# Kernel tuning notes

Hardware: AMD Instinct MI355X
Metric: run time of the kernel (lower is better)

The kernel has to match this reference:

```python
import jax, jax.numpy as jnp
import numpy as np

B, A, N, P, D, H = 2, 9, 1024, 4, 256, 8
DH = D // H
EPS = 1e-12


def _layernorm(x, gamma, beta):
    m = jnp.mean(x, axis=-1, keepdims=True)
    v = jnp.var(x, axis=-1, keepdims=True)
    return (x - m) / jnp.sqrt(v + EPS) * gamma + beta


def setup_inputs() -> dict:
    key = jax.random.key(0)
    ks = jax.random.split(key, 10)
    # adjacency stacks A relation matrices; scale 1/N keeps the P-step matmul chain O(1)
    adjacency = jax.random.uniform(ks[0], (B, A, N, N), jnp.float32) / N
    # diagonal, strictly positive degree matrix -> invertible
    diag = 1.0 + jax.random.uniform(ks[1], (B, N), jnp.float32)
    degree = jax.vmap(jnp.diag)(diag)
    x = jax.random.normal(ks[2], (B, N, D), jnp.float32)
    # per-head params stacked on leading H axis
    kernels = 0.1 * jax.random.normal(ks[3], (H, A, P), jnp.float32)  # RandomNormal(0, 0.1)
    lim = np.sqrt(6.0 / D).astype(np.float32)
    Wv = jax.random.uniform(ks[4], (H, D, DH), jnp.float32, -lim, lim)  # he_uniform
    Bv = jnp.zeros((H, N, DH), jnp.float32)
    W0 = jax.random.uniform(ks[5], (D, D), jnp.float32, -lim, lim)
    gamma2 = jnp.ones((D,), jnp.float32)
    beta2 = jnp.zeros((D,), jnp.float32)
    W1 = jax.random.normal(ks[6], (D, 2 * D), jnp.float32) * np.sqrt(2.0 / D).astype(np.float32)
    b1 = jnp.zeros((2 * D,), jnp.float32)
    gf = jnp.ones((2 * D,), jnp.float32)
    bf = jnp.zeros((2 * D,), jnp.float32)
    W2 = jax.random.normal(ks[7], (2 * D, D), jnp.float32) * np.sqrt(2.0 / (2 * D)).astype(np.float32)
    b2f = jnp.zeros((D,), jnp.float32)
    return {"adjacency": adjacency, "degree": degree, "x": x, "kernels": kernels,
            "Wv": Wv, "Bv": Bv, "W0": W0, "gamma2": gamma2, "beta2": beta2,
            "W1": W1, "b1": b1, "gf": gf, "bf": bf, "W2": W2, "b2f": b2f}


def reference(adjacency, degree, x, kernels, Wv, Bv, W0, gamma2, beta2, W1, b1, gf, bf, W2, b2f):
    # ---- AdjacencyAggregator (all H heads batched on leading axis) ----
    # softmax(relu(kernel)) over the input-channel (relation) axis
    soft = jax.nn.softmax(jax.nn.relu(kernels), axis=-2)  # [H, A, P]
    # 1x1 conv == per-position convex mix of the A relation matrices, one mix per path step
    # sequential chain: meta = M_0 @ M_1 @ ... @ M_{P-1}   (P is small and fixed)
    result = jnp.einsum('banm,ha->hbnm', adjacency, soft[:, :, 0])  # [H, B, N, N]
    for i in range(1, P):
        mi = jnp.einsum('banm,ha->hbnm', adjacency, soft[:, :, i])
        result = jnp.matmul(result, mi)
    inv_deg = jnp.linalg.inv(degree)                # [B, N, N], shared across heads
    normed = jnp.matmul(inv_deg[None], result)      # [H, B, N, N]
    # ---- MetaPathHead value projection + message passing ----
    V = jnp.einsum('bnd,hde->hbne', x, Wv) + Bv[:, None]   # [H, B, N, DH]
    heads = jnp.matmul(normed, V)                          # [H, B, N, DH]
    # concat along feature axis in head order
    attn = jnp.transpose(heads, (1, 2, 0, 3)).reshape(B, N, D)
    # ---- outer block: W0, residual, pre-norm FFN ----
    residual = attn @ W0 + x
    h = _layernorm(residual, gamma2, beta2)
    f = jax.nn.gelu(h @ W1 + b1, approximate=False)
    f = _layernorm(f, gf, bf)
    out = f @ W2 + b2f + residual
    return out
```

## Files before the change

kernel.cpp:

```cpp
#include <hip/hip_runtime.h>
#include <hip/hip_bf16.h>
#include <math.h>

#define B_ 2
#define A_ 9
#define N_ 1024
#define P_ 4
#define D_ 256
#define H_ 8
#define DH_ 32
#define ROWS_ (B_*N_)
#define KS_ 8
#define ADJ_ELEMS_ ((size_t)B_*A_*N_*N_)
#define SLABF4_ 131072

typedef __attribute__((ext_vector_type(8))) short bf16x8;
typedef __attribute__((ext_vector_type(4))) float f32x4;

__device__ __forceinline__ uint pack2_bf(float x, float y) {
    uint ux = __float_as_uint(x); ux += 0x7fffu + ((ux >> 16) & 1u);
    uint uy = __float_as_uint(y); uy += 0x7fffu + ((uy >> 16) & 1u);
    return (ux >> 16) | (uy & 0xffff0000u);
}
__device__ __forceinline__ float bflo(uint u){ return __uint_as_float(u << 16); }
__device__ __forceinline__ float bfhi(uint u){ return __uint_as_float(u & 0xffff0000u); }

__global__ void prep_kernel(const float* __restrict__ kernels, const float* __restrict__ degree,
                            float* __restrict__ soft, float* __restrict__ invd)
{
    int t = threadIdx.x;
    if (blockIdx.x == 0) {
        if (t < H_*P_) {
            int h = t >> 2, p = t & 3;
            float vals[A_];
            float m = 0.0f;
            #pragma unroll
            for (int a = 0; a < A_; a++) {
                float v = kernels[h*A_*P_ + a*P_ + p];
                v = v > 0.0f ? v : 0.0f;
                vals[a] = v;
                m = fmaxf(m, v);
            }
            float s = 0.0f;
            #pragma unroll
            for (int a = 0; a < A_; a++) { vals[a] = expf(vals[a] - m); s += vals[a]; }
            float inv = 1.0f / s;
            #pragma unroll
            for (int a = 0; a < A_; a++) soft[h*A_*P_ + a*P_ + p] = vals[a] * inv;
        }
    } else {
        int idx = (blockIdx.x - 1) * 256 + t;
        if (idx < ROWS_) {
            int b = idx >> 10, n = idx & (N_-1);
            invd[idx] = 1.0f / degree[(size_t)b*N_*N_ + (size_t)n*N_ + n];
        }
    }
}

__global__ void adj_pack_kernel(const float* __restrict__ in, ushort* __restrict__ out)
{
    int j = blockIdx.x * 256 + threadIdx.x;
    int kk8   = j & 3;
    int r     = (j >> 2) & 15;
    int t     = j >> 6;
    int a     = t % 9;
    int rest  = t / 9;
    int chunk = rest & 3;
    int ks    = (rest >> 2) & 7;
    int rowblk= (rest >> 5) & 63;
    int b     = rest >> 11;
    const float* src = &in[(((size_t)b*A_ + a)*N_ + (rowblk*16 + r))*N_ + ks*128 + chunk*32 + kk8*8];
    float4 v0 = *(const float4*)src;
    float4 v1 = *(const float4*)(src + 4);
    uint4 o;
    o.x = pack2_bf(v0.x, v0.y);
    o.y = pack2_bf(v0.z, v0.w);
    o.z = pack2_bf(v1.x, v1.y);
    o.w = pack2_bf(v1.z, v1.w);
    ((uint4*)out)[j] = o;
}

__global__ __launch_bounds__(256, 4)
void chain_mfma(const ushort* __restrict__ adjp, const float* __restrict__ soft,
                const ushort* __restrict__ Tin, float* __restrict__ Pp, int step)
{
    __shared__ __align__(16) ushort smem[8*640 + 16*648];
    __shared__ float soft_s[8][9];
    ushort* sm_ms = smem;
    ushort* sm_t  = smem + 8*640;

    int bid    = blockIdx.x;
    int ks     = bid & (KS_-1);
    int rowblk = (bid >> 3) & 63;
    int b      = bid >> 9;
    int n0     = rowblk * 16;
    int tid    = threadIdx.x;
    int lane   = tid & 63;
    int w      = tid >> 6;

    if (tid < 72) { int h = tid/9, a = tid%9; soft_s[h][a] = soft[h*A_*P_ + a*P_ + step]; }
    __syncthreads();

    int mr   = tid >> 4;
    int mk2  = (tid & 15) * 2;
    int mk2s = mk2 ^ ((mr & 3) << 3);
    const ushort* ablk = adjp + (size_t)((b*64 + rowblk)*8 + ks) * 18432;

    int sp  = tid >> 4;
    int sk0 = (tid & 15) * 2;
    const ushort* tbase = Tin + ((size_t)(b*16 + sp)*1024 + (size_t)ks*128) * 16;

    int g   = lane >> 4;
    int c15 = lane & 15;
    int gx  = (g ^ (c15 & 3)) * 8;

    f32x4 acc[4];
    #pragma unroll
    for (int j = 0; j < 4; j++) acc[j] = (f32x4){0.f, 0.f, 0.f, 0.f};

    for (int chunk = 0; chunk < 4; chunk++) {
        uint av[9];
        {
            const ushort* asl = ablk + chunk*4608 + mk2;
            #pragma unroll
            for (int a = 0; a < A_; a++) av[a] = *(const uint*)&asl[(a*16 + mr)*32];
        }
        const ushort* tsl = tbase + (size_t)(chunk*32 + sk0) * 16;
        uint4 q0 = *(const uint4*)(tsl + 0);
        uint4 q1 = *(const uint4*)(tsl + 8);
        uint4 q2 = *(const uint4*)(tsl + 16);
        uint4 q3 = *(const uint4*)(tsl + 24);

        if (chunk) __syncthreads();

        {
            float va0[9], va1[9];
            #pragma unroll
            for (int a = 0; a < A_; a++) { va0[a] = bflo(av[a]); va1[a] = bfhi(av[a]); }
            #pragma unroll
            for (int h = 0; h < H_; h++) {
                float s0 = soft_s[h][0]*va0[0];
                float s1 = soft_s[h][0]*va1[0];
                #pragma unroll
                for (int a = 1; a < A_; a++) { s0 += soft_s[h][a]*va0[a]; s1 += soft_s[h][a]*va1[a]; }
                *(uint*)&sm_ms[h*640 + mr*40 + mk2s] = pack2_bf(s0, s1);
            }
        }
        {
            uint l0[4] = {q0.x, q0.y, q0.z, q0.w};
            uint l1[4] = {q1.x, q1.y, q1.z, q1.w};
            uint h0[4] = {q2.x, q2.y, q2.z, q2.w};
            uint h1[4] = {q3.x, q3.y, q3.z, q3.w};
            #pragma unroll
            for (int ci = 0; ci < 8; ci++) {
                uint a0 = (l0[ci>>1] >> ((ci&1)*16)) & 0xffffu;
                uint b0 = (h0[ci>>1] >> ((ci&1)*16)) & 0xffffu;
                int k0s = sk0 ^ ((ci & 3) << 3);
                *(uint*)&sm_t[sp*648 + ci*40 + k0s] = a0 | (b0 << 16);
            }
            #pragma unroll
            for (int ci = 0; ci < 8; ci++) {
                int c = ci + 8;
                uint a0 = (l1[ci>>1] >> ((ci&1)*16)) & 0xffffu;
                uint b0 = (h1[ci>>1] >> ((ci&1)*16)) & 0xffffu;
                int k0s = sk0 ^ ((c & 3) << 3);
                *(uint*)&sm_t[sp*648 + c*40 + k0s] = a0 | (b0 << 16);
            }
        }
        __syncthreads();

        {
            const ushort* mb = sm_ms + c15*40 + gx;
            const ushort* tb = sm_t  + c15*40 + gx;
            #pragma unroll
            for (int j = 0; j < 4; j++) {
                int cg = w + 4*j;
                int h  = cg >> 1;
                bf16x8 af  = *(const bf16x8*)&mb[h*640];
                bf16x8 bfr = *(const bf16x8*)&tb[cg*648];
                acc[j] = __builtin_amdgcn_mfma_f32_16x16x32_bf16(af, bfr, acc[j], 0, 0, 0);
            }
        }
    }

    __syncthreads();
    float* Ep = (float*)smem;
    #pragma unroll
    for (int j = 0; j < 4; j++) {
        int cg = w + 4*j;
        #pragma unroll
        for (int i = 0; i < 4; i++)
            Ep[cg*256 + (g*4 + i)*16 + c15] = acc[j][i];
    }
    __syncthreads();
    {
        int p = tid >> 4, r = tid & 15;
        float* dst = Pp + (((size_t)(ks*B_ + b)*16 + p)*N_ + (n0 + r)) * 16;
        const float* src = &Ep[p*256 + r*16];
        *(float4*)&dst[0]  = *(const float4*)&src[0];
        *(float4*)&dst[4]  = *(const float4*)&src[4];
        *(float4*)&dst[8]  = *(const float4*)&src[8];
        *(float4*)&dst[12] = *(const float4*)&src[12];
    }
}

template<int FINAL>
__global__ void chain_reduce(const float* __restrict__ Pp, ushort* __restrict__ outp,
                             const float* __restrict__ invd)
{
    int pidx = blockIdx.x * 256 + threadIdx.x;
    float4 s = make_float4(0.f, 0.f, 0.f, 0.f);
    #pragma unroll
    for (int ks = 0; ks < KS_; ks++) {
        float4 v = ((const float4*)Pp)[(size_t)ks*SLABF4_ + pidx];
        s.x += v.x; s.y += v.y; s.z += v.z; s.w += v.w;
    }
    if constexpr (FINAL) {
        int lin = pidx * 4;
        int n  = (lin >> 4) & (N_-1);
        int b  = lin >> 18;
        float sc = invd[b*N_ + n];
        s.x *= sc; s.y *= sc; s.z *= sc; s.w *= sc;
    }
    uint2 wv;
    wv.x = pack2_bf(s.x, s.y);
    wv.y = pack2_bf(s.z, s.w);
    ((uint2*)outp)[pidx] = wv;
}

#define BK 16
__global__ void gemm_v(const float* __restrict__ A, const float* __restrict__ Bm,
                       const float* __restrict__ bias, ushort* __restrict__ C)
{
    __shared__ __align__(16) float As[BK][68];
    __shared__ __align__(16) float Bs[BK][68];
    int m0 = blockIdx.x * 64;
    int n0 = blockIdx.y * 64;
    int tid = threadIdx.x;
    int tx = tid & 15, ty = tid >> 4;

    float acc[4][4];
    #pragma unroll
    for (int i = 0; i < 4; i++)
        #pragma unroll
        for (int j = 0; j < 4; j++) acc[i][j] = 0.0f;

    for (int k0 = 0; k0 < D_; k0 += BK) {
        {
            int m = tid >> 2;
            int k = (tid & 3) * 4;
            float4 v = *(const float4*)&A[(size_t)(m0+m)*D_ + k0 + k];
            As[k+0][m] = v.x; As[k+1][m] = v.y; As[k+2][m] = v.z; As[k+3][m] = v.w;
        }
        {
            int k = tid >> 4;
            int n = (tid & 15) * 4;
            int c = n0 + n; int h = c >> 5; int ee = c & 31;
            float4 v = *(const float4*)&Bm[(size_t)h*D_*DH_ + (size_t)(k0+k)*DH_ + ee];
            *(float4*)&Bs[k][n] = v;
        }
        __syncthreads();
        #pragma unroll
        for (int k = 0; k < BK; k++) {
            float4 a4 = *(const float4*)&As[k][ty*4];
            float4 b4 = *(const float4*)&Bs[k][tx*4];
            acc[0][0] += a4.x*b4.x; acc[0][1] += a4.x*b4.y; acc[0][2] += a4.x*b4.z; acc[0][3] += a4.x*b4.w;
            acc[1][0] += a4.y*b4.x; acc[1][1] += a4.y*b4.y; acc[1][2] += a4.y*b4.z; acc[1][3] += a4.y*b4.w;
            acc[2][0] += a4.z*b4.x; acc[2][1] += a4.z*b4.y; acc[2][2] += a4.z*b4.z; acc[2][3] += a4.z*b4.w;
            acc[3][0] += a4.w*b4.x; acc[3][1] += a4.w*b4.y; acc[3][2] += a4.w*b4.z; acc[3][3] += a4.w*b4.w;
        }
        __syncthreads();
    }

    #pragma unroll
    for (int i = 0; i < 4; i++) {
        int row  = m0 + ty*4 + i;
        int nloc = n0 + tx*4;
        float o[4];
        #pragma unroll
        for (int j = 0; j < 4; j++) {
            int c = nloc + j;
            int h = c >> 5, ee = c & 31, n = row & (N_-1);
            o[j] = acc[i][j] + bias[(size_t)h*N_*DH_ + (size_t)n*DH_ + ee];
        }
        int bb = row >> 10, n = row & (N_-1);
        int cg = nloc >> 4, cc = nloc & 15;
        uint2 wv;
        wv.x = pack2_bf(o[0], o[1]);
        wv.y = pack2_bf(o[2], o[3]);
        *(uint2*)&C[(((size_t)bb*16 + cg)*N_ + n)*16 + cc] = wv;
    }
}


__global__ __launch_bounds__(256, 2)
void gemm_r(const ushort* __restrict__ attnp, const float* __restrict__ W0,
            const float* __restrict__ x, const float* __restrict__ gamma,
            const float* __restrict__ beta, float* __restrict__ resid,
            ushort* __restrict__ hbuf)
{
    __shared__ __align__(16) ushort As[16*40];
    __shared__ __align__(16) ushort Bs[256*40];
    __shared__ float lnb[16*257];
    __shared__ float2 stat[16];

    int m0 = blockIdx.x * 16;
    int b16 = (m0 >> 10) * 16;
    int nb  = m0 & (N_-1);
    int tid = threadIdx.x;
    int lane = tid & 63;
    int w = tid >> 6;
    int g = lane >> 4, c15 = lane & 15;
    int gx = (g ^ (c15 & 3)) * 8;

    int am = tid >> 4, ak2 = (tid & 15) * 2;
    int apos = am*40 + ((((ak2>>3) ^ (am&3))) << 3) + (ak2 & 7);
    int bn8 = (tid & 31) * 8;
    int bkq = (tid >> 5) * 4;
    int bpos0 = (((bkq>>3)) << 3) + (bkq & 7);

    f32x4 acc[4];
    #pragma unroll
    for (int j = 0; j < 4; j++) acc[j] = (f32x4){0.f,0.f,0.f,0.f};

    for (int ks = 0; ks < 8; ks++) {
        int k0 = ks * 32;
        int k = k0 + ak2;
        uint av = *(const uint*)&attnp[(((size_t)(b16 + (k>>4)))*N_ + nb + am)*16 + (k & 15)];
        float4 lo[4], hi[4];
        #pragma unroll
        for (int i = 0; i < 4; i++) {
            lo[i] = *(const float4*)&W0[(size_t)(k0+bkq+i)*D_ + bn8];
            hi[i] = *(const float4*)&W0[(size_t)(k0+bkq+i)*D_ + bn8 + 4];
        }
        if (ks) __syncthreads();
        *(uint*)&As[apos] = av;
        #pragma unroll
        for (int jn = 0; jn < 8; jn++) {
            int n = bn8 + jn;
            float v0 = (jn<4)? ((const float*)&lo[0])[jn] : ((const float*)&hi[0])[jn-4];
            float v1 = (jn<4)? ((const float*)&lo[1])[jn] : ((const float*)&hi[1])[jn-4];
            float v2 = (jn<4)? ((const float*)&lo[2])[jn] : ((const float*)&hi[2])[jn-4];
            float v3 = (jn<4)? ((const float*)&lo[3])[jn] : ((const float*)&hi[3])[jn-4];
            uint2 wv; wv.x = pack2_bf(v0, v1); wv.y = pack2_bf(v2, v3);
            *(uint2*)&Bs[n*40 + (bpos0 ^ ((n&3)<<3))] = wv;
        }
        __syncthreads();
        const ushort* ab = As + c15*40 + gx;
        #pragma unroll
        for (int nt = 0; nt < 4; nt++) {
            int n = w*64 + nt*16 + c15;
            bf16x8 af  = *(const bf16x8*)ab;
            bf16x8 bfr = *(const bf16x8*)&Bs[n*40 + gx];
            acc[nt] = __builtin_amdgcn_mfma_f32_16x16x32_bf16(af, bfr, acc[nt], 0, 0, 0);
        }
    }
    __syncthreads();

    #pragma unroll
    for (int nt = 0; nt < 4; nt++) {
        int c = w*64 + nt*16 + c15;
        #pragma unroll
        for (int i = 0; i < 4; i++) {
            int r = g*4 + i;
            lnb[r*257 + c] = acc[nt][i] + x[(size_t)(m0+r)*D_ + c];
        }
    }
    __syncthreads();

    {
        int rr = tid >> 4, sl = tid & 15;
        float sum = 0.f, sq = 0.f;
        #pragma unroll
        for (int j = 0; j < 16; j++) {
            float v = lnb[rr*257 + sl + 16*j];
            sum += v; sq += v*v;
        }
        #pragma unroll
        for (int m = 1; m < 16; m <<= 1) { sum += __shfl_xor(sum, m); sq += __shfl_xor(sq, m); }
        if (sl == 0) {
            float mean = sum * (1.0f/D_);
            float var  = fmaxf(sq * (1.0f/D_) - mean*mean, 0.f);
            stat[rr] = make_float2(mean, rsqrtf(var + 1e-12f));
        }
    }
    __syncthreads();

    {
        int rr = tid & 15, s2 = tid >> 4;
        float2 ms = stat[rr];
        int c0 = s2 * 16;
        uint hw[8];
        #pragma unroll
        for (int q = 0; q < 4; q++) {
            int c = c0 + q*4;
            float4 v = *(const float4*)&lnb[rr*257 + c];
            *(float4*)&resid[(size_t)(m0+rr)*D_ + c] = v;
            float4 gm = *(const float4*)&gamma[c];
            float4 bt = *(const float4*)&beta[c];
            float h0 = (v.x - ms.x)*ms.y*gm.x + bt.x;
            float h1 = (v.y - ms.x)*ms.y*gm.y + bt.y;
            float h2 = (v.z - ms.x)*ms.y*gm.z + bt.z;
            float h3 = (v.w - ms.x)*ms.y*gm.w + bt.w;
            hw[2*q]   = pack2_bf(h0, h1);
            hw[2*q+1] = pack2_bf(h2, h3);
        }
        ushort* hp = &hbuf[(size_t)(m0+rr)*D_ + c0];
        *(uint4*)&hp[0] = make_uint4(hw[0], hw[1], hw[2], hw[3]);
        *(uint4*)&hp[8] = make_uint4(hw[4], hw[5], hw[6], hw[7]);
    }
}

__global__ __launch_bounds__(256, 2)
void gemm_f1(const ushort* __restrict__ hbuf, const float* __restrict__ W1,
             const float* __restrict__ b1, const float* __restrict__ gf,
             const float* __restrict__ bfv, ushort* __restrict__ fout)
{
    __shared__ __align__(16) ushort As[16*40];
    __shared__ __align__(16) ushort Bs[512*40];
    __shared__ float lnb[16*513];
    __shared__ float2 stat[16];

    int m0 = blockIdx.x * 16;
    int tid = threadIdx.x;
    int lane = tid & 63;
    int w = tid >> 6;
    int g = lane >> 4, c15 = lane & 15;
    int gx = (g ^ (c15 & 3)) * 8;

    int am = tid >> 4, ak2 = (tid & 15) * 2;
    int apos = am*40 + ((((ak2>>3) ^ (am&3))) << 3) + (ak2 & 7);
    int bn8 = (tid & 63) * 8;
    int bk8 = (tid >> 6) * 8;

    f32x4 acc[8];
    #pragma unroll
    for (int j = 0; j < 8; j++) acc[j] = (f32x4){0.f,0.f,0.f,0.f};

    for (int ks = 0; ks < 8; ks++) {
        int k0 = ks * 32;
        uint av = *(const uint*)&hbuf[(size_t)(m0+am)*D_ + k0 + ak2];
        float4 q[16];
        #pragma unroll
        for (int i = 0; i < 8; i++) {
            q[2*i]   = *(const float4*)&W1[(size_t)(k0+bk8+i)*(2*D_) + bn8];
            q[2*i+1] = *(const float4*)&W1[(size_t)(k0+bk8+i)*(2*D_) + bn8 + 4];
        }
        if (ks) __syncthreads();
        *(uint*)&As[apos] = av;
        #pragma unroll
        for (int jn = 0; jn < 8; jn++) {
            int n = bn8 + jn;
            float e0 = (jn<4)? ((const float*)&q[0])[jn]  : ((const float*)&q[1])[jn-4];
            float e1 = (jn<4)? ((const float*)&q[2])[jn]  : ((const float*)&q[3])[jn-4];
            float e2 = (jn<4)? ((const float*)&q[4])[jn]  : ((const float*)&q[5])[jn-4];
            float e3 = (jn<4)? ((const float*)&q[6])[jn]  : ((const float*)&q[7])[jn-4];
            float e4 = (jn<4)? ((const float*)&q[8])[jn]  : ((const float*)&q[9])[jn-4];
            float e5 = (jn<4)? ((const float*)&q[10])[jn] : ((const float*)&q[11])[jn-4];
            float e6 = (jn<4)? ((const float*)&q[12])[jn] : ((const float*)&q[13])[jn-4];
            float e7 = (jn<4)? ((const float*)&q[14])[jn] : ((const float*)&q[15])[jn-4];
            uint4 wv;
            wv.x = pack2_bf(e0, e1); wv.y = pack2_bf(e2, e3);
            wv.z = pack2_bf(e4, e5); wv.w = pack2_bf(e6, e7);
            *(uint4*)&Bs[n*40 + ((((bk8>>3) ^ (n&3))) << 3)] = wv;
        }
        __syncthreads();
        const ushort* ab = As + c15*40 + gx;
        #pragma unroll
        for (int nt = 0; nt < 8; nt++) {
            int n = w*128 + nt*16 + c15;
            bf16x8 af  = *(const bf16x8*)ab;
            bf16x8 bfr = *(const bf16x8*)&Bs[n*40 + gx];
            acc[nt] = __builtin_amdgcn_mfma_f32_16x16x32_bf16(af, bfr, acc[nt], 0, 0, 0);
        }
    }
    __syncthreads();

    #pragma unroll
    for (int nt = 0; nt < 8; nt++) {
        int c = w*128 + nt*16 + c15;
        float bias = b1[c];
        #pragma unroll
        for (int i = 0; i < 4; i++) {
            int r = g*4 + i;
            float v = acc[nt][i] + bias;
            v = 0.5f * v * (1.0f + erff(v * 0.70710678118654752f));
            lnb[r*513 + c] = v;
        }
    }
    __syncthreads();

    {
        int rr = tid >> 4, sl = tid & 15;
        float sum = 0.f, sq = 0.f;
        #pragma unroll
        for (int j = 0; j < 32; j++) {
            float v = lnb[rr*513 + sl + 16*j];
            sum += v; sq += v*v;
        }
        #pragma unroll
        for (int m = 1; m < 16; m <<= 1) { sum += __shfl_xor(sum, m); sq += __shfl_xor(sq, m); }
        if (sl == 0) {
            float mean = sum * (1.0f/(2*D_));
            float var  = fmaxf(sq * (1.0f/(2*D_)) - mean*mean, 0.f);
            stat[rr] = make_float2(mean, rsqrtf(var + 1e-12f));
        }
    }
    __syncthreads();

    {
        int rr = tid & 15, s2 = tid >> 4;
        float2 ms = stat[rr];
        int c0 = s2 * 32;
        #pragma unroll
        for (int q = 0; q < 8; q++) {
            int c = c0 + q*4;
            float4 v = *(const float4*)&lnb[rr*513 + c];
            float4 gm = *(const float4*)&gf[c];
            float4 bt = *(const float4*)&bfv[c];
            float h0 = (v.x - ms.x)*ms.y*gm.x + bt.x;
            float h1 = (v.y - ms.x)*ms.y*gm.y + bt.y;
            float h2 = (v.z - ms.x)*ms.y*gm.z + bt.z;
            float h3 = (v.w - ms.x)*ms.y*gm.w + bt.w;
            *(uint2*)&fout[(size_t)(m0+rr)*(2*D_) + c] = make_uint2(pack2_bf(h0,h1), pack2_bf(h2,h3));
        }
    }
}

__global__ __launch_bounds__(256, 2)
void gemm_f2(const ushort* __restrict__ fbuf, const float* __restrict__ W2,
             const float* __restrict__ b2f, const float* __restrict__ resid,
             float* __restrict__ outp)
{
    __shared__ __align__(16) ushort As[16*40];
    __shared__ __align__(16) ushort Bs[256*40];
    __shared__ float lnb[16*257];

    int m0 = blockIdx.x * 16;
    int tid = threadIdx.x;
    int lane = tid & 63;
    int w = tid >> 6;
    int g = lane >> 4, c15 = lane & 15;
    int gx = (g ^ (c15 & 3)) * 8;

    int am = tid >> 4, ak2 = (tid & 15) * 2;
    int apos = am*40 + ((((ak2>>3) ^ (am&3))) << 3) + (ak2 & 7);
    int bn8 = (tid & 31) * 8;
    int bkq = (tid >> 5) * 4;
    int bpos0 = (((bkq>>3)) << 3) + (bkq & 7);

    f32x4 acc[4];
    #pragma unroll
    for (int j = 0; j < 4; j++) acc[j] = (f32x4){0.f,0.f,0.f,0.f};

    for (int ks = 0; ks < 16; ks++) {
        int k0 = ks * 32;
        uint av = *(const uint*)&fbuf[(size_t)(m0+am)*(2*D_) + k0 + ak2];
        float4 lo[4], hi[4];
        #pragma unroll
        for (int i = 0; i < 4; i++) {
            lo[i] = *(const float4*)&W2[(size_t)(k0+bkq+i)*D_ + bn8];
            hi[i] = *(const float4*)&W2[(size_t)(k0+bkq+i)*D_ + bn8 + 4];
        }
        if (ks) __syncthreads();
        *(uint*)&As[apos] = av;
        #pragma unroll
        for (int jn = 0; jn < 8; jn++) {
            int n = bn8 + jn;
            float v0 = (jn<4)? ((const float*)&lo[0])[jn] : ((const float*)&hi[0])[jn-4];
            float v1 = (jn<4)? ((const float*)&lo[1])[jn] : ((const float*)&hi[1])[jn-4];
            float v2 = (jn<4)? ((const float*)&lo[2])[jn] : ((const float*)&hi[2])[jn-4];
            float v3 = (jn<4)? ((const float*)&lo[3])[jn] : ((const float*)&hi[3])[jn-4];
            uint2 wv; wv.x = pack2_bf(v0, v1); wv.y = pack2_bf(v2, v3);
            *(uint2*)&Bs[n*40 + (bpos0 ^ ((n&3)<<3))] = wv;
        }
        __syncthreads();
        const ushort* ab = As + c15*40 + gx;
        #pragma unroll
        for (int nt = 0; nt < 4; nt++) {
            int n = w*64 + nt*16 + c15;
            bf16x8 af  = *(const bf16x8*)ab;
            bf16x8 bfr = *(const bf16x8*)&Bs[n*40 + gx];
            acc[nt] = __builtin_amdgcn_mfma_f32_16x16x32_bf16(af, bfr, acc[nt], 0, 0, 0);
        }
    }
    __syncthreads();

    #pragma unroll
    for (int nt = 0; nt < 4; nt++) {
        int c = w*64 + nt*16 + c15;
        #pragma unroll
        for (int i = 0; i < 4; i++)
            lnb[(g*4+i)*257 + c] = acc[nt][i];
    }
    __syncthreads();

    {
        int rr = tid & 15, s2 = tid >> 4;
        int c0 = s2 * 16;
        #pragma unroll
        for (int q = 0; q < 4; q++) {
            int c = c0 + q*4;
            float4 v  = *(const float4*)&lnb[rr*257 + c];
            float4 bb = *(const float4*)&b2f[c];
            float4 rs = *(const float4*)&resid[(size_t)(m0+rr)*D_ + c];
            float4 o = make_float4(v.x+bb.x+rs.x, v.y+bb.y+rs.y, v.z+bb.z+rs.z, v.w+bb.w+rs.w);
            *(float4*)&outp[(size_t)(m0+rr)*D_ + c] = o;
        }
    }
}

extern "C" void kernel_launch(void* const* d_in, const int* in_sizes, int n_in,
                              void* d_out, int out_size, void* d_ws, size_t ws_size,
                              hipStream_t stream)
{
    const float* adj    = (const float*)d_in[0];
    const float* degree = (const float*)d_in[1];
    const float* x      = (const float*)d_in[2];
    const float* kern   = (const float*)d_in[3];
    const float* Wv     = (const float*)d_in[4];
    const float* Bv     = (const float*)d_in[5];
    const float* W0     = (const float*)d_in[6];
    const float* gamma2 = (const float*)d_in[7];
    const float* beta2  = (const float*)d_in[8];
    const float* W1     = (const float*)d_in[9];
    const float* b1     = (const float*)d_in[10];
    const float* gf     = (const float*)d_in[11];
    const float* bf_    = (const float*)d_in[12];
    const float* W2     = (const float*)d_in[13];
    const float* b2f    = (const float*)d_in[14];
    float* out = (float*)d_out;
    float* ws  = (float*)d_ws;

    size_t off = 0;
    float* soft  = ws + off; off += 512;
    float* invd  = ws + off; off += 2048;
    float* T0    = ws + off; off += (size_t)ROWS_*D_;
    float* T1    = ws + off; off += (size_t)ROWS_*D_;
    float* resid = ws + off; off += (size_t)ROWS_*D_;
    float* hbuf  = ws + off; off += (size_t)ROWS_*D_;
    float* fbuf  = ws + off; off += (size_t)ROWS_*2*D_;
    float* fbuf2 = ws + off; off += (size_t)ROWS_*2*D_;
    float* Pp    = ws + off; off += (size_t)KS_*ROWS_*D_;
    ushort* adjp = (ushort*)(ws + off);
    (void)fbuf2;

    ushort* T0b = (ushort*)T0;
    ushort* T1b = (ushort*)T1;
    ushort* hb  = (ushort*)hbuf;
    ushort* fb  = (ushort*)fbuf;

    prep_kernel<<<9, 256, 0, stream>>>(kern, degree, soft, invd);
    adj_pack_kernel<<<(int)(ADJ_ELEMS_/8/256), 256, 0, stream>>>(adj, adjp);
    gemm_v<<<dim3(ROWS_/64, D_/64), 256, 0, stream>>>(x, Wv, Bv, T0b);

    int chain_grid  = B_*64*KS_;
    int reduce_grid = SLABF4_/256;
    chain_mfma<<<chain_grid, 256, 0, stream>>>(adjp, soft, T0b, Pp, 3);
    chain_reduce<0><<<reduce_grid, 256, 0, stream>>>(Pp, T1b, invd);
    chain_mfma<<<chain_grid, 256, 0, stream>>>(adjp, soft, T1b, Pp, 2);
    chain_reduce<0><<<reduce_grid, 256, 0, stream>>>(Pp, T0b, invd);
    chain_mfma<<<chain_grid, 256, 0, stream>>>(adjp, soft, T0b, Pp, 1);
    chain_reduce<0><<<reduce_grid, 256, 0, stream>>>(Pp, T1b, invd);
    chain_mfma<<<chain_grid, 256, 0, stream>>>(adjp, soft, T1b, Pp, 0);
    chain_reduce<1><<<reduce_grid, 256, 0, stream>>>(Pp, T0b, invd);

    gemm_r <<<ROWS_/16, 256, 0, stream>>>(T0b, W0, x, gamma2, beta2, resid, hb);
    gemm_f1<<<ROWS_/16, 256, 0, stream>>>(hb, W1, b1, gf, bf_, fb);
    gemm_f2<<<ROWS_/16, 256, 0, stream>>>(fb, W2, b2f, resid, out);
}
```

Baseline: 200.5 us.

## Fuse adjacency packing into first chain step and fuse final reduce with FFN

Result: faster. 195.1 us (-2.7%).

```diff
diff --git a/kernel.cpp b/kernel.cpp
--- a/kernel.cpp
+++ b/kernel.cpp
@@ -12,7 +12,8 @@
 #define ROWS_ (B_*N_)
 #define KS_ 8
 #define ADJ_ELEMS_ ((size_t)B_*A_*N_*N_)
-#define SLABF4_ 131072
+#define SLABF_ 524288
+#define SLABF4_ (SLABF_/4)
 
 typedef __attribute__((ext_vector_type(8))) short bf16x8;
 typedef __attribute__((ext_vector_type(4))) float f32x4;
@@ -22,8 +23,13 @@
     uint uy = __float_as_uint(y); uy += 0x7fffu + ((uy >> 16) & 1u);
     return (ux >> 16) | (uy & 0xffff0000u);
 }
+__device__ __forceinline__ ushort bf1(float v) {
+    uint u = __float_as_uint(v); u += 0x7fffu + ((u >> 16) & 1u);
+    return (ushort)(u >> 16);
+}
 __device__ __forceinline__ float bflo(uint u){ return __uint_as_float(u << 16); }
 __device__ __forceinline__ float bfhi(uint u){ return __uint_as_float(u & 0xffff0000u); }
+__device__ __forceinline__ float bfs(ushort u){ return __uint_as_float((uint)u << 16); }
 
 __global__ void prep_kernel(const float* __restrict__ kernels, const float* __restrict__ degree,
                             float* __restrict__ soft, float* __restrict__ invd)
@@ -57,31 +63,10 @@
     }
 }
 
-__global__ void adj_pack_kernel(const float* __restrict__ in, ushort* __restrict__ out)
-{
-    int j = blockIdx.x * 256 + threadIdx.x;
-    int kk8   = j & 3;
-    int r     = (j >> 2) & 15;
-    int t     = j >> 6;
-    int a     = t % 9;
-    int rest  = t / 9;
-    int chunk = rest & 3;
-    int ks    = (rest >> 2) & 7;
-    int rowblk= (rest >> 5) & 63;
-    int b     = rest >> 11;
-    const float* src = &in[(((size_t)b*A_ + a)*N_ + (rowblk*16 + r))*N_ + ks*128 + chunk*32 + kk8*8];
-    float4 v0 = *(const float4*)src;
-    float4 v1 = *(const float4*)(src + 4);
-    uint4 o;
-    o.x = pack2_bf(v0.x, v0.y);
-    o.y = pack2_bf(v0.z, v0.w);
-    o.z = pack2_bf(v1.x, v1.y);
-    o.w = pack2_bf(v1.z, v1.w);
-    ((uint4*)out)[j] = o;
-}
-
+template<int PACK>
 __global__ __launch_bounds__(256, 4)
-void chain_mfma(const ushort* __restrict__ adjp, const float* __restrict__ soft,
+void chain_mfma(const float* __restrict__ adjf, ushort* __restrict__ adjp,
+                const float* __restrict__ soft,
                 const ushort* __restrict__ Tin, float* __restrict__ Pp, int step)
 {
     __shared__ __align__(16) ushort smem[8*640 + 16*648];
@@ -104,7 +89,7 @@
     int mr   = tid >> 4;
     int mk2  = (tid & 15) * 2;
     int mk2s = mk2 ^ ((mr & 3) << 3);
-    const ushort* ablk = adjp + (size_t)((b*64 + rowblk)*8 + ks) * 18432;
+    ushort* ablk = adjp + (size_t)((b*64 + rowblk)*8 + ks) * 18432;
 
     int sp  = tid >> 4;
     int sk0 = (tid & 15) * 2;
@@ -119,11 +104,20 @@
     for (int j = 0; j < 4; j++) acc[j] = (f32x4){0.f, 0.f, 0.f, 0.f};
 
     for (int chunk = 0; chunk < 4; chunk++) {
-        uint av[9];
-        {
-            const ushort* asl = ablk + chunk*4608 + mk2;
-            #pragma unroll
-            for (int a = 0; a < A_; a++) av[a] = *(const uint*)&asl[(a*16 + mr)*32];
+        float lo[9], hi[9];
+        if constexpr (PACK) {
+            #pragma unroll
+            for (int a = 0; a < A_; a++) {
+                float2 v = *(const float2*)&adjf[(((size_t)b*A_ + a)*N_ + (n0+mr))*N_
+                                                 + ks*128 + chunk*32 + mk2];
+                lo[a] = v.x; hi[a] = v.y;
+            }
+        } else {
+            #pragma unroll
+            for (int a = 0; a < A_; a++) {
+                uint av = *(const uint*)&ablk[chunk*4608 + (a*16 + mr)*32 + mk2];
+                lo[a] = bflo(av); hi[a] = bfhi(av);
+            }
         }
         const ushort* tsl = tbase + (size_t)(chunk*32 + sk0) * 16;
         uint4 q0 = *(const uint4*)(tsl + 0);
@@ -131,20 +125,21 @@
         uint4 q2 = *(const uint4*)(tsl + 16);
         uint4 q3 = *(const uint4*)(tsl + 24);
 
+        if constexpr (PACK) {
+            #pragma unroll
+            for (int a = 0; a < A_; a++)
+                *(uint*)&ablk[chunk*4608 + (a*16 + mr)*32 + mk2] = pack2_bf(lo[a], hi[a]);
+        }
+
         if (chunk) __syncthreads();
 
-        {
-            float va0[9], va1[9];
-            #pragma unroll
-            for (int a = 0; a < A_; a++) { va0[a] = bflo(av[a]); va1[a] = bfhi(av[a]); }
-            #pragma unroll
-            for (int h = 0; h < H_; h++) {
-                float s0 = soft_s[h][0]*va0[0];
-                float s1 = soft_s[h][0]*va1[0];
-                #pragma unroll
-                for (int a = 1; a < A_; a++) { s0 += soft_s[h][a]*va0[a]; s1 += soft_s[h][a]*va1[a]; }
-                *(uint*)&sm_ms[h*640 + mr*40 + mk2s] = pack2_bf(s0, s1);
-            }
+        #pragma unroll
+        for (int h = 0; h < H_; h++) {
+            float s0 = soft_s[h][0]*lo[0];
+            float s1 = soft_s[h][0]*hi[0];
+            #pragma unroll
+            for (int a = 1; a < A_; a++) { s0 += soft_s[h][a]*lo[a]; s1 += soft_s[h][a]*hi[a]; }
+            *(uint*)&sm_ms[h*640 + mr*40 + mk2s] = pack2_bf(s0, s1);
         }
         {
             uint l0[4] = {q0.x, q0.y, q0.z, q0.w};
@@ -204,9 +199,7 @@
     }
 }
 
-template<int FINAL>
-__global__ void chain_reduce(const float* __restrict__ Pp, ushort* __restrict__ outp,
-                             const float* __restrict__ invd)
+__global__ void chain_reduce(const float* __restrict__ Pp, ushort* __restrict__ outp)
 {
     int pidx = blockIdx.x * 256 + threadIdx.x;
     float4 s = make_float4(0.f, 0.f, 0.f, 0.f);
@@ -214,13 +207,6 @@
     for (int ks = 0; ks < KS_; ks++) {
         float4 v = ((const float4*)Pp)[(size_t)ks*SLABF4_ + pidx];
         s.x += v.x; s.y += v.y; s.z += v.z; s.w += v.w;
-    }
-    if constexpr (FINAL) {
-        int lin = pidx * 4;
-        int n  = (lin >> 4) & (N_-1);
-        int b  = lin >> 18;
-        float sc = invd[b*N_ + n];
-        s.x *= sc; s.y *= sc; s.z *= sc; s.w *= sc;
     }
     uint2 wv;
     wv.x = pack2_bf(s.x, s.y);
@@ -292,20 +278,26 @@
     }
 }
 
-
-__global__ __launch_bounds__(256, 2)
-void gemm_r(const ushort* __restrict__ attnp, const float* __restrict__ W0,
-            const float* __restrict__ x, const float* __restrict__ gamma,
-            const float* __restrict__ beta, float* __restrict__ resid,
-            ushort* __restrict__ hbuf)
+__global__ __launch_bounds__(512, 1)
+void ffn_fused(const float* __restrict__ Pp, const float* __restrict__ invd,
+               const float* __restrict__ W0, const float* __restrict__ x,
+               const float* __restrict__ gamma, const float* __restrict__ beta,
+               const float* __restrict__ W1, const float* __restrict__ b1,
+               const float* __restrict__ gf, const float* __restrict__ bfv,
+               const float* __restrict__ W2, const float* __restrict__ b2f,
+               float* __restrict__ outp)
 {
-    __shared__ __align__(16) ushort As[16*40];
-    __shared__ __align__(16) ushort Bs[256*40];
-    __shared__ float lnb[16*257];
-    __shared__ float2 stat[16];
-
-    int m0 = blockIdx.x * 16;
-    int b16 = (m0 >> 10) * 16;
+    __shared__ __align__(16) ushort arena[41760];
+    ushort* As  = arena;
+    ushort* Bs  = arena + 640;
+    ushort* hL  = arena + 21120;
+    ushort* fL  = arena + 25216;
+    float*  lnb = (float*)(arena + 33408);
+    float2* statR = (float2*)(arena + 41632);
+    float2* statF = statR + 16;
+
+    int m0  = blockIdx.x * 16;
+    int b   = m0 >> 10;
     int nb  = m0 & (N_-1);
     int tid = threadIdx.x;
     int lane = tid & 63;
@@ -313,62 +305,69 @@
     int g = lane >> 4, c15 = lane & 15;
     int gx = (g ^ (c15 & 3)) * 8;
 
-    int am = tid >> 4, ak2 = (tid & 15) * 2;
+    int am  = tid >> 4;
+    int ak2 = (tid & 15) * 2;
     int apos = am*40 + ((((ak2>>3) ^ (am&3))) << 3) + (ak2 & 7);
-    int bn8 = (tid & 31) * 8;
-    int bkq = (tid >> 5) * 4;
-    int bpos0 = (((bkq>>3)) << 3) + (bkq & 7);
-
-    f32x4 acc[4];
-    #pragma unroll
-    for (int j = 0; j < 4; j++) acc[j] = (f32x4){0.f,0.f,0.f,0.f};
-
-    for (int ks = 0; ks < 8; ks++) {
-        int k0 = ks * 32;
-        int k = k0 + ak2;
-        uint av = *(const uint*)&attnp[(((size_t)(b16 + (k>>4)))*N_ + nb + am)*16 + (k & 15)];
-        float4 lo[4], hi[4];
-        #pragma unroll
-        for (int i = 0; i < 4; i++) {
-            lo[i] = *(const float4*)&W0[(size_t)(k0+bkq+i)*D_ + bn8];
-            hi[i] = *(const float4*)&W0[(size_t)(k0+bkq+i)*D_ + bn8 + 4];
-        }
-        if (ks) __syncthreads();
-        *(uint*)&As[apos] = av;
-        #pragma unroll
-        for (int jn = 0; jn < 8; jn++) {
-            int n = bn8 + jn;
-            float v0 = (jn<4)? ((const float*)&lo[0])[jn] : ((const float*)&hi[0])[jn-4];
-            float v1 = (jn<4)? ((const float*)&lo[1])[jn] : ((const float*)&hi[1])[jn-4];
-            float v2 = (jn<4)? ((const float*)&lo[2])[jn] : ((const float*)&hi[2])[jn-4];
-            float v3 = (jn<4)? ((const float*)&lo[3])[jn] : ((const float*)&hi[3])[jn-4];
-            uint2 wv; wv.x = pack2_bf(v0, v1); wv.y = pack2_bf(v2, v3);
-            *(uint2*)&Bs[n*40 + (bpos0 ^ ((n&3)<<3))] = wv;
-        }
-        __syncthreads();
-        const ushort* ab = As + c15*40 + gx;
-        #pragma unroll
-        for (int nt = 0; nt < 4; nt++) {
-            int n = w*64 + nt*16 + c15;
-            bf16x8 af  = *(const bf16x8*)ab;
-            bf16x8 bfr = *(const bf16x8*)&Bs[n*40 + gx];
-            acc[nt] = __builtin_amdgcn_mfma_f32_16x16x32_bf16(af, bfr, acc[nt], 0, 0, 0);
-        }
-    }
-    __syncthreads();
-
-    #pragma unroll
-    for (int nt = 0; nt < 4; nt++) {
-        int c = w*64 + nt*16 + c15;
+    float idv = 0.f;
+    if (tid < 256) idv = invd[b*N_ + nb + am];
+
+    f32x4 accR[2];
+    accR[0] = (f32x4){0.f,0.f,0.f,0.f};
+    accR[1] = (f32x4){0.f,0.f,0.f,0.f};
+    {
+        int n8  = (tid & 31) * 8;
+        int kq2 = (tid >> 5) * 2;
+        int bposR = ((kq2 >> 3) << 3) + (kq2 & 7);
+        for (int ksi = 0; ksi < 8; ksi++) {
+            int k0 = ksi * 32;
+            uint av = 0;
+            if (tid < 256) {
+                int k = k0 + ak2;
+                size_t base = (((size_t)(b*16 + (k>>4)))*N_ + nb + am)*16 + (k & 15);
+                float s0 = 0.f, s1 = 0.f;
+                #pragma unroll
+                for (int sl = 0; sl < 8; sl++) {
+                    float2 v = *(const float2*)&Pp[(size_t)sl*SLABF_ + base];
+                    s0 += v.x; s1 += v.y;
+                }
+                av = pack2_bf(s0*idv, s1*idv);
+            }
+            float4 r0a = *(const float4*)&W0[(size_t)(k0+kq2  )*D_ + n8];
+            float4 r0b = *(const float4*)&W0[(size_t)(k0+kq2  )*D_ + n8 + 4];
+            float4 r1a = *(const float4*)&W0[(size_t)(k0+kq2+1)*D_ + n8];
+            float4 r1b = *(const float4*)&W0[(size_t)(k0+kq2+1)*D_ + n8 + 4];
+            if (ksi) __syncthreads();
+            if (tid < 256) *(uint*)&As[apos] = av;
+            #pragma unroll
+            for (int jn = 0; jn < 8; jn++) {
+                int n = n8 + jn;
+                float v0 = (jn<4)? ((const float*)&r0a)[jn] : ((const float*)&r0b)[jn-4];
+                float v1 = (jn<4)? ((const float*)&r1a)[jn] : ((const float*)&r1b)[jn-4];
+                *(uint*)&Bs[n*40 + (bposR ^ ((n&3)<<3))] = pack2_bf(v0, v1);
+            }
+            __syncthreads();
+            const ushort* ab = As + c15*40 + gx;
+            #pragma unroll
+            for (int nt = 0; nt < 2; nt++) {
+                int n = (w*2 + nt)*16 + c15;
+                bf16x8 af  = *(const bf16x8*)ab;
+                bf16x8 bfr = *(const bf16x8*)&Bs[n*40 + gx];
+                accR[nt] = __builtin_amdgcn_mfma_f32_16x16x32_bf16(af, bfr, accR[nt], 0, 0, 0);
+            }
+        }
+    }
+    __syncthreads();
+    #pragma unroll
+    for (int nt = 0; nt < 2; nt++) {
+        int c = (w*2 + nt)*16 + c15;
         #pragma unroll
         for (int i = 0; i < 4; i++) {
             int r = g*4 + i;
-            lnb[r*257 + c] = acc[nt][i] + x[(size_t)(m0+r)*D_ + c];
-        }
-    }
-    __syncthreads();
-
-    {
+            lnb[r*257 + c] = accR[nt][i] + x[(size_t)(m0+r)*D_ + c];
+        }
+    }
+    __syncthreads();
+    if (tid < 256) {
         int rr = tid >> 4, sl = tid & 15;
         float sum = 0.f, sq = 0.f;
         #pragma unroll
@@ -381,21 +380,19 @@
         if (sl == 0) {
             float mean = sum * (1.0f/D_);
             float var  = fmaxf(sq * (1.0f/D_) - mean*mean, 0.f);
-            stat[rr] = make_float2(mean, rsqrtf(var + 1e-12f));
-        }
-    }
-    __syncthreads();
-
-    {
+            statR[rr] = make_float2(mean, rsqrtf(var + 1e-12f));
+        }
+    }
+    __syncthreads();
+    if (tid < 256) {
         int rr = tid & 15, s2 = tid >> 4;
-        float2 ms = stat[rr];
+        float2 ms = statR[rr];
         int c0 = s2 * 16;
         uint hw[8];
         #pragma unroll
         for (int q = 0; q < 4; q++) {
             int c = c0 + q*4;
             float4 v = *(const float4*)&lnb[rr*257 + c];
-            *(float4*)&resid[(size_t)(m0+rr)*D_ + c] = v;
             float4 gm = *(const float4*)&gamma[c];
             float4 bt = *(const float4*)&beta[c];
             float h0 = (v.x - ms.x)*ms.y*gm.x + bt.x;
@@ -405,97 +402,72 @@
             hw[2*q]   = pack2_bf(h0, h1);
             hw[2*q+1] = pack2_bf(h2, h3);
         }
-        ushort* hp = &hbuf[(size_t)(m0+rr)*D_ + c0];
-        *(uint4*)&hp[0] = make_uint4(hw[0], hw[1], hw[2], hw[3]);
-        *(uint4*)&hp[8] = make_uint4(hw[4], hw[5], hw[6], hw[7]);
-    }
-}
-
-__global__ __launch_bounds__(256, 2)
-void gemm_f1(const ushort* __restrict__ hbuf, const float* __restrict__ W1,
-             const float* __restrict__ b1, const float* __restrict__ gf,
-             const float* __restrict__ bfv, ushort* __restrict__ fout)
-{
-    __shared__ __align__(16) ushort As[16*40];
-    __shared__ __align__(16) ushort Bs[512*40];
-    __shared__ float lnb[16*513];
-    __shared__ float2 stat[16];
-
-    int m0 = blockIdx.x * 16;
-    int tid = threadIdx.x;
-    int lane = tid & 63;
-    int w = tid >> 6;
-    int g = lane >> 4, c15 = lane & 15;
-    int gx = (g ^ (c15 & 3)) * 8;
-
-    int am = tid >> 4, ak2 = (tid & 15) * 2;
-    int apos = am*40 + ((((ak2>>3) ^ (am&3))) << 3) + (ak2 & 7);
-    int bn8 = (tid & 63) * 8;
-    int bk8 = (tid >> 6) * 8;
-
-    f32x4 acc[8];
-    #pragma unroll
-    for (int j = 0; j < 8; j++) acc[j] = (f32x4){0.f,0.f,0.f,0.f};
-
-    for (int ks = 0; ks < 8; ks++) {
-        int k0 = ks * 32;
-        uint av = *(const uint*)&hbuf[(size_t)(m0+am)*D_ + k0 + ak2];
-        float4 q[16];
-        #pragma unroll
-        for (int i = 0; i < 8; i++) {
-            q[2*i]   = *(const float4*)&W1[(size_t)(k0+bk8+i)*(2*D_) + bn8];
-            q[2*i+1] = *(const float4*)&W1[(size_t)(k0+bk8+i)*(2*D_) + bn8 + 4];
-        }
-        if (ks) __syncthreads();
-        *(uint*)&As[apos] = av;
-        #pragma unroll
-        for (int jn = 0; jn < 8; jn++) {
-            int n = bn8 + jn;
-            float e0 = (jn<4)? ((const float*)&q[0])[jn]  : ((const float*)&q[1])[jn-4];
-            float e1 = (jn<4)? ((const float*)&q[2])[jn]  : ((const float*)&q[3])[jn-4];
-            float e2 = (jn<4)? ((const float*)&q[4])[jn]  : ((const float*)&q[5])[jn-4];
-            float e3 = (jn<4)? ((const float*)&q[6])[jn]  : ((const float*)&q[7])[jn-4];
-            float e4 = (jn<4)? ((const float*)&q[8])[jn]  : ((const float*)&q[9])[jn-4];
-            float e5 = (jn<4)? ((const float*)&q[10])[jn] : ((const float*)&q[11])[jn-4];
-            float e6 = (jn<4)? ((const float*)&q[12])[jn] : ((const float*)&q[13])[jn-4];
-            float e7 = (jn<4)? ((const float*)&q[14])[jn] : ((const float*)&q[15])[jn-4];
-            uint4 wv;
-            wv.x = pack2_bf(e0, e1); wv.y = pack2_bf(e2, e3);
-            wv.z = pack2_bf(e4, e5); wv.w = pack2_bf(e6, e7);
-            *(uint4*)&Bs[n*40 + ((((bk8>>3) ^ (n&3))) << 3)] = wv;
-        }
-        __syncthreads();
-        const ushort* ab = As + c15*40 + gx;
-        #pragma unroll
-        for (int nt = 0; nt < 8; nt++) {
-            int n = w*128 + nt*16 + c15;
-            bf16x8 af  = *(const bf16x8*)ab;
-            bf16x8 bfr = *(const bf16x8*)&Bs[n*40 + gx];
-            acc[nt] = __builtin_amdgcn_mfma_f32_16x16x32_bf16(af, bfr, acc[nt], 0, 0, 0);
-        }
-    }
-    __syncthreads();
-
-    #pragma unroll
-    for (int nt = 0; nt < 8; nt++) {
-        int c = w*128 + nt*16 + c15;
+        *(uint4*)&hL[rr*256 + c0    ] = make_uint4(hw[0], hw[1], hw[2], hw[3]);
+        *(uint4*)&hL[rr*256 + c0 + 8] = make_uint4(hw[4], hw[5], hw[6], hw[7]);
+    }
+    __syncthreads();
+
+    f32x4 acc1[4];
+    #pragma unroll
+    for (int j = 0; j < 4; j++) acc1[j] = (f32x4){0.f,0.f,0.f,0.f};
+    {
+        int n8  = (tid & 63) * 8;
+        int kq4 = (tid >> 6) * 4;
+        for (int ksi = 0; ksi < 8; ksi++) {
+            int k0 = ksi * 32;
+            uint av = 0;
+            if (tid < 256) av = *(const uint*)&hL[am*256 + k0 + ak2];
+            float4 q0a = *(const float4*)&W1[(size_t)(k0+kq4  )*(2*D_) + n8];
+            float4 q0b = *(const float4*)&W1[(size_t)(k0+kq4  )*(2*D_) + n8 + 4];
+            float4 q1a = *(const float4*)&W1[(size_t)(k0+kq4+1)*(2*D_) + n8];
+            float4 q1b = *(const float4*)&W1[(size_t)(k0+kq4+1)*(2*D_) + n8 + 4];
+            float4 q2a = *(const float4*)&W1[(size_t)(k0+kq4+2)*(2*D_) + n8];
+            float4 q2b = *(const float4*)&W1[(size_t)(k0+kq4+2)*(2*D_) + n8 + 4];
+            float4 q3a = *(const float4*)&W1[(size_t)(k0+kq4+3)*(2*D_) + n8];
+            float4 q3b = *(const float4*)&W1[(size_t)(k0+kq4+3)*(2*D_) + n8 + 4];
+            __syncthreads();
+            if (tid < 256) *(uint*)&As[apos] = av;
+            #pragma unroll
+            for (int jn = 0; jn < 8; jn++) {
+                int n = n8 + jn;
+                float e0 = (jn<4)? ((const float*)&q0a)[jn] : ((const float*)&q0b)[jn-4];
+                float e1 = (jn<4)? ((const float*)&q1a)[jn] : ((const float*)&q1b)[jn-4];
+                float e2 = (jn<4)? ((const float*)&q2a)[jn] : ((const float*)&q2b)[jn-4];
+                float e3 = (jn<4)? ((const float*)&q3a)[jn] : ((const float*)&q3b)[jn-4];
+                int pos = ((((kq4>>3) ^ (n&3))) << 3) + (kq4 & 7);
+                *(uint2*)&Bs[n*40 + pos] = make_uint2(pack2_bf(e0,e1), pack2_bf(e2,e3));
+            }
+            __syncthreads();
+            const ushort* ab = As + c15*40 + gx;
+            #pragma unroll
+            for (int nt = 0; nt < 4; nt++) {
+                int n = (w*4 + nt)*16 + c15;
+                bf16x8 af  = *(const bf16x8*)ab;
+                bf16x8 bfr = *(const bf16x8*)&Bs[n*40 + gx];
+                acc1[nt] = __builtin_amdgcn_mfma_f32_16x16x32_bf16(af, bfr, acc1[nt], 0, 0, 0);
+            }
+        }
+    }
+    __syncthreads();
+    #pragma unroll
+    for (int nt = 0; nt < 4; nt++) {
+        int c = (w*4 + nt)*16 + c15;
         float bias = b1[c];
         #pragma unroll
         for (int i = 0; i < 4; i++) {
             int r = g*4 + i;
-            float v = acc[nt][i] + bias;
+            float v = acc1[nt][i] + bias;
             v = 0.5f * v * (1.0f + erff(v * 0.70710678118654752f));
-            lnb[r*513 + c] = v;
-        }
-    }
-    __syncthreads();
-
-    {
+            fL[r*512 + c] = bf1(v);
+        }
+    }
+    __syncthreads();
+    if (tid < 256) {
         int rr = tid >> 4, sl = tid & 15;
         float sum = 0.f, sq = 0.f;
         #pragma unroll
         for (int j = 0; j < 32; j++) {
-            float v = lnb[rr*513 + sl + 16*j];
+            float v = bfs(fL[rr*512 + sl + 16*j]);
             sum += v; sq += v*v;
         }
         #pragma unroll
@@ -503,109 +475,85 @@
         if (sl == 0) {
             float mean = sum * (1.0f/(2*D_));
             float var  = fmaxf(sq * (1.0f/(2*D_)) - mean*mean, 0.f);
-            stat[rr] = make_float2(mean, rsqrtf(var + 1e-12f));
-        }
-    }
-    __syncthreads();
-
-    {
+            statF[rr] = make_float2(mean, rsqrtf(var + 1e-12f));
+        }
+    }
+    __syncthreads();
+    if (tid < 256) {
         int rr = tid & 15, s2 = tid >> 4;
-        float2 ms = stat[rr];
+        float2 ms = statF[rr];
         int c0 = s2 * 32;
         #pragma unroll
         for (int q = 0; q < 8; q++) {
             int c = c0 + q*4;
-            float4 v = *(const float4*)&lnb[rr*513 + c];
-            float4 gm = *(const float4*)&gf[c];
-            float4 bt = *(const float4*)&bfv[c];
-            float h0 = (v.x - ms.x)*ms.y*gm.x + bt.x;
-            float h1 = (v.y - ms.x)*ms.y*gm.y + bt.y;
-            float h2 = (v.z - ms.x)*ms.y*gm.z + bt.z;
-            float h3 = (v.w - ms.x)*ms.y*gm.w + bt.w;
-            *(uint2*)&fout[(size_t)(m0+rr)*(2*D_) + c] = make_uint2(pack2_bf(h0,h1), pack2_bf(h2,h3));
-        }
-    }
-}
-
-__global__ __launch_bounds__(256, 2)
-void gemm_f2(const ushort* __restrict__ fbuf, const float* __restrict__ W2,
-             const float* __restrict__ b2f, const float* __restrict__ resid,
-             float* __restrict__ outp)
-{
-    __shared__ __align__(16) ushort As[16*40];
-    __shared__ __align__(16) ushort Bs[256*40];
-    __shared__ float lnb[16*257];
-
-    int m0 = blockIdx.x * 16;
-    int tid = threadIdx.x;
-    int lane = tid & 63;
-    int w = tid >> 6;
-    int g = lane >> 4, c15 = lane & 15;
-    int gx = (g ^ (c15 & 3)) * 8;
-
-    int am = tid >> 4, ak2 = (tid & 15) * 2;
-    int apos = am*40 + ((((ak2>>3) ^ (am&3))) << 3) + (ak2 & 7);
-    int bn8 = (tid & 31) * 8;
-    int bkq = (tid >> 5) * 4;
-    int bpos0 = (((bkq>>3)) << 3) + (bkq & 7);
-
-    f32x4 acc[4];
-    #pragma unroll
-    for (int j = 0; j < 4; j++) acc[j] = (f32x4){0.f,0.f,0.f,0.f};
-
-    for (int ks = 0; ks < 16; ks++) {
-        int k0 = ks * 32;
-        uint av = *(const uint*)&fbuf[(size_t)(m0+am)*(2*D_) + k0 + ak2];
-        float4 lo[4], hi[4];
-        #pragma unroll
-        for (int i = 0; i < 4; i++) {
-            lo[i] = *(const float4*)&W2[(size_t)(k0+bkq+i)*D_ + bn8];
-            hi[i] = *(const float4*)&W2[(size_t)(k0+bkq+i)*D_ + bn8 + 4];
-        }
-        if (ks) __syncthreads();
-        *(uint*)&As[apos] = av;
-        #pragma unroll
-        for (int jn = 0; jn < 8; jn++) {
-            int n = bn8 + jn;
-            float v0 = (jn<4)? ((const float*)&lo[0])[jn] : ((const float*)&hi[0])[jn-4];
-            float v1 = (jn<4)? ((const float*)&lo[1])[jn] : ((const float*)&hi[1])[jn-4];
-            float v2 = (jn<4)? ((const float*)&lo[2])[jn] : ((const float*)&hi[2])[jn-4];
-            float v3 = (jn<4)? ((const float*)&lo[3])[jn] : ((const float*)&hi[3])[jn-4];
-            uint2 wv; wv.x = pack2_bf(v0, v1); wv.y = pack2_bf(v2, v3);
-            *(uint2*)&Bs[n*40 + (bpos0 ^ ((n&3)<<3))] = wv;
+            uint2 u = *(const uint2*)&fL[rr*512 + c];
+            float v0 = (bflo(u.x) - ms.x)*ms.y*gf[c+0] + bfv[c+0];
+            float v1 = (bfhi(u.x) - ms.x)*ms.y*gf[c+1] + bfv[c+1];
+            float v2 = (bflo(u.y) - ms.x)*ms.y*gf[c+2] + bfv[c+2];
+            float v3 = (bfhi(u.y) - ms.x)*ms.y*gf[c+3] + bfv[c+3];
+            *(uint2*)&fL[rr*512 + c] = make_uint2(pack2_bf(v0,v1), pack2_bf(v2,v3));
+        }
+    }
+    __syncthreads();
+
+    f32x4 acc2[2];
+    acc2[0] = (f32x4){0.f,0.f,0.f,0.f};
+    acc2[1] = (f32x4){0.f,0.f,0.f,0.f};
+    {
+        int n8  = (tid & 31) * 8;
+        int kq2 = (tid >> 5) * 2;
+        int bposR = ((kq2 >> 3) << 3) + (kq2 & 7);
+        for (int ksi = 0; ksi < 16; ksi++) {
+            int k0 = ksi * 32;
+            uint av = 0;
+            if (tid < 256) av = *(const uint*)&fL[am*512 + k0 + ak2];
+            float4 r0a = *(const float4*)&W2[(size_t)(k0+kq2  )*D_ + n8];
+            float4 r0b = *(const float4*)&W2[(size_t)(k0+kq2  )*D_ + n8 + 4];
+            float4 r1a = *(const float4*)&W2[(size_t)(k0+kq2+1)*D_ + n8];
+            float4 r1b = *(const float4*)&W2[(size_t)(k0+kq2+1)*D_ + n8 + 4];
+            __syncthreads();
+            if (tid < 256) *(uint*)&As[apos] = av;
+            #pragma unroll
+            for (int jn = 0; jn < 8; jn++) {
+                int n = n8 + jn;
+                float v0 = (jn<4)? ((const float*)&r0a)[jn] : ((const float*)&r0b)[jn-4];
+                float v1 = (jn<4)? ((const float*)&r1a)[jn] : ((const float*)&r1b)[jn-4];
+                *(uint*)&Bs[n*40 + (bposR ^ ((n&3)<<3))] = pack2_bf(v0, v1);
+            }
+            __syncthreads();
+            const ushort* ab = As + c15*40 + gx;
+            #pragma unroll
+            for (int nt = 0; nt < 2; nt++) {
+                int n = (w*2 + nt)*16 + c15;
+                bf16x8 af  = *(const bf16x8*)ab;
+                bf16x8 bfr = *(const bf16x8*)&Bs[n*40 + gx];
+                acc2[nt] = __builtin_amdgcn_mfma_f32_16x16x32_bf16(af, bfr, acc2[nt], 0, 0, 0);
+            }
+        }
+    }
+    __syncthreads();
+    {
+        float* esc = (float*)(arena + 640);
+        #pragma unroll
+        for (int nt = 0; nt < 2; nt++) {
+            int c = (w*2 + nt)*16 + c15;
+            #pragma unroll
+            for (int i = 0; i < 4; i++)
+                esc[(g*4+i)*257 + c] = acc2[nt][i];
         }
         __syncthreads();
-        const ushort* ab = As + c15*40 + gx;
-        #pragma unroll
-        for (int nt = 0; nt < 4; nt++) {
-            int n = w*64 + nt*16 + c15;
-            bf16x8 af  = *(const bf16x8*)ab;
-            bf16x8 bfr = *(const bf16x8*)&Bs[n*40 + gx];
-            acc[nt] = __builtin_amdgcn_mfma_f32_16x16x32_bf16(af, bfr, acc[nt], 0, 0, 0);
-        }
-    }
-    __syncthreads();
-
-    #pragma unroll
-    for (int nt = 0; nt < 4; nt++) {
-        int c = w*64 + nt*16 + c15;
-        #pragma unroll
-        for (int i = 0; i < 4; i++)
-            lnb[(g*4+i)*257 + c] = acc[nt][i];
-    }
-    __syncthreads();
-
-    {
-        int rr = tid & 15, s2 = tid >> 4;
-        int c0 = s2 * 16;
-        #pragma unroll
-        for (int q = 0; q < 4; q++) {
-            int c = c0 + q*4;
-            float4 v  = *(const float4*)&lnb[rr*257 + c];
-            float4 bb = *(const float4*)&b2f[c];
-            float4 rs = *(const float4*)&resid[(size_t)(m0+rr)*D_ + c];
-            float4 o = make_float4(v.x+bb.x+rs.x, v.y+bb.y+rs.y, v.z+bb.z+rs.z, v.w+bb.w+rs.w);
-            *(float4*)&outp[(size_t)(m0+rr)*D_ + c] = o;
+        if (tid < 256) {
+            int rr = tid & 15, s2 = tid >> 4;
+            int c0 = s2 * 16;
+            #pragma unroll
+            for (int q = 0; q < 4; q++) {
+                int c = c0 + q*4;
+                float4 v  = *(const float4*)&esc[rr*257 + c];
+                float4 bb = *(const float4*)&b2f[c];
+                float4 rs = *(const float4*)&lnb[rr*257 + c];
+                float4 o = make_float4(v.x+bb.x+rs.x, v.y+bb.y+rs.y, v.z+bb.z+rs.z, v.w+bb.w+rs.w);
+                *(float4*)&outp[(size_t)(m0+rr)*D_ + c] = o;
+            }
         }
     }
 }
@@ -637,35 +585,24 @@
     float* invd  = ws + off; off += 2048;
     float* T0    = ws + off; off += (size_t)ROWS_*D_;
     float* T1    = ws + off; off += (size_t)ROWS_*D_;
-    float* resid = ws + off; off += (size_t)ROWS_*D_;
-    float* hbuf  = ws + off; off += (size_t)ROWS_*D_;
-    float* fbuf  = ws + off; off += (size_t)ROWS_*2*D_;
-    float* fbuf2 = ws + off; off += (size_t)ROWS_*2*D_;
     float* Pp    = ws + off; off += (size_t)KS_*ROWS_*D_;
     ushort* adjp = (ushort*)(ws + off);
-    (void)fbuf2;
 
     ushort* T0b = (ushort*)T0;
     ushort* T1b = (ushort*)T1;
-    ushort* hb  = (ushort*)hbuf;
-    ushort* fb  = (ushort*)fbuf;
 
     prep_kernel<<<9, 256, 0, stream>>>(kern, degree, soft, invd);
-    adj_pack_kernel<<<(int)(ADJ_ELEMS_/8/256), 256, 0, stream>>>(adj, adjp);
     gemm_v<<<dim3(ROWS_/64, D_/64), 256, 0, stream>>>(x, Wv, Bv, T0b);
 
     int chain_grid  = B_*64*KS_;
     int reduce_grid = SLABF4_/256;
-    chain_mfma<<<chain_grid, 256, 0, stream>>>(adjp, soft, T0b, Pp, 3);
-    chain_reduce<0><<<reduce_grid, 256, 0, stream>>>(Pp, T1b, invd);
-    chain_mfma<<<chain_grid, 256, 0, stream>>>(adjp, soft, T1b, Pp, 2);
-    chain_reduce<0><<<reduce_grid, 256, 0, stream>>>(Pp, T0b, invd);
-    chain_mfma<<<chain_grid, 256, 0, stream>>>(adjp, soft, T0b, Pp, 1);
-    chain_reduce<0><<<reduce_grid, 256, 0, stream>>>(Pp, T1b, invd);
-    chain_mfma<<<chain_grid, 256, 0, stream>>>(adjp, soft, T1b, Pp, 0);
-    chain_reduce<1><<<reduce_grid, 256, 0, stream>>>(Pp, T0b, invd);
-
-    gemm_r <<<ROWS_/16, 256, 0, stream>>>(T0b, W0, x, gamma2, beta2, resid, hb);
-    gemm_f1<<<ROWS_/16, 256, 0, stream>>>(hb, W1, b1, gf, bf_, fb);
-    gemm_f2<<<ROWS_/16, 256, 0, stream>>>(fb, W2, b2f, resid, out);
-}
+    chain_mfma<1><<<chain_grid, 256, 0, stream>>>(adj, adjp, soft, T0b, Pp, 3);
+    chain_reduce<<<reduce_grid, 256, 0, stream>>>(Pp, T1b);
+    chain_mfma<0><<<chain_grid, 256, 0, stream>>>(adj, adjp, soft, T1b, Pp, 2);
+    chain_reduce<<<reduce_grid, 256, 0, stream>>>(Pp, T0b);
+    chain_mfma<0><<<chain_grid, 256, 0, stream>>>(adj, adjp, soft, T0b, Pp, 1);
+    chain_reduce<<<reduce_grid, 256, 0, stream>>>(Pp, T1b);
+    chain_mfma<0><<<chain_grid, 256, 0, stream>>>(adj, adjp, soft, T1b, Pp, 0);
+    ffn_fused<<<ROWS_/16, 512, 0, stream>>>(Pp, invd, W0, x, gamma2, beta2,
+                                            W1, b1, gf, bf_, W2, b2f, out);
+}
```
